# Kernel optimization log

Hardware: AMD Instinct MI355X
Metric: run time of the kernel (lower is better)

## Reference

```python
import jax, jax.numpy as jnp
import numpy as np

NUM_NODES = 200000
NUM_EDGES = 200000
NUM_GRAPHS = 2048
F_IN = 128
H = 64


def setup_inputs() -> dict:
    key = jax.random.key(0)
    ks = jax.random.split(key, 16)
    x = jax.random.normal(ks[0], (NUM_NODES, F_IN), dtype=jnp.float32)
    edge_index = jax.random.randint(ks[1], (2, NUM_EDGES), 0, NUM_NODES, dtype=jnp.int64)
    batch = jnp.sort(jax.random.randint(ks[2], (NUM_NODES,), 0, NUM_GRAPHS, dtype=jnp.int64))
    s_in = 1.0 / np.sqrt(F_IN)
    s_h = 1.0 / np.sqrt(H)
    W1a = jax.random.uniform(ks[3], (F_IN, H), jnp.float32, -s_in, s_in)
    b1a = jax.random.uniform(ks[4], (H,), jnp.float32, -s_in, s_in)
    W1b = jax.random.uniform(ks[5], (H, H), jnp.float32, -s_h, s_h)
    b1b = jax.random.uniform(ks[6], (H,), jnp.float32, -s_h, s_h)
    W2a = jax.random.uniform(ks[7], (H, H), jnp.float32, -s_h, s_h)
    b2a = jax.random.uniform(ks[8], (H,), jnp.float32, -s_h, s_h)
    W2b = jax.random.uniform(ks[9], (H, H), jnp.float32, -s_h, s_h)
    b2b = jax.random.uniform(ks[10], (H,), jnp.float32, -s_h, s_h)
    fcW = jax.random.uniform(ks[11], (H, 1), jnp.float32, -s_h, s_h)
    fcb = jax.random.uniform(ks[12], (1,), jnp.float32, -s_h, s_h)
    return {"x": x, "edge_index": edge_index, "batch": batch,
            "W1a": W1a, "b1a": b1a, "W1b": W1b, "b1b": b1b,
            "W2a": W2a, "b2a": b2a, "W2b": W2b, "b2b": b2b,
            "fcW": fcW, "fcb": fcb}


def gin_conv(h, edge_index, Wa, ba, Wb, bb):
    # sum aggregation: messages from source (row 0) scattered to target (row 1)
    msgs = h[edge_index[0]]  # [E, D]
    agg = jax.ops.segment_sum(msgs, edge_index[1], num_segments=NUM_NODES)
    z = h + agg  # eps = 0 default: (1+eps)*x + sum_j x_j
    z = jnp.maximum(z @ Wa + ba, 0.0)
    return z @ Wb + bb


def reference(x, edge_index, batch, W1a, b1a, W1b, b1b, W2a, b2a, W2b, b2b, fcW, fcb):
    h = jnp.maximum(gin_conv(x, edge_index, W1a, b1a, W1b, b1b), 0.0)
    h = jnp.maximum(gin_conv(h, edge_index, W2a, b2a, W2b, b2b), 0.0)
    # global mean pool per graph
    sums = jax.ops.segment_sum(h, batch, num_segments=NUM_GRAPHS)  # [G, H]
    counts = jax.ops.segment_sum(jnp.ones((h.shape[0],), h.dtype), batch, num_segments=NUM_GRAPHS)
    pooled = sums / jnp.maximum(counts, 1.0)[:, None]
    out = pooled @ fcW + fcb  # [G, 1]
    return out.squeeze(-1)
```

## Files before the change

kernel.cpp:

```cpp
#include <hip/hip_runtime.h>
#include <hip/hip_bf16.h>


#define NODES 200000
#define EDGES 200000
#define GRAPHS 2048
#define NB_SCAN 782

typedef __attribute__((ext_vector_type(8))) short short8;
typedef __attribute__((ext_vector_type(4))) float f32x4;

__device__ __forceinline__ unsigned short f2bf(float f) {
    unsigned u = __builtin_bit_cast(unsigned, f);
    u = (u + 0x7fffu + ((u >> 16) & 1u)) >> 16;
    return (unsigned short)u;
}
__device__ __forceinline__ float bf2f(unsigned short h) {
    unsigned u = ((unsigned)h) << 16;
    return __builtin_bit_cast(float, u);
}

__global__ __launch_bounds__(256) void count_k(
    const int* __restrict__ ei, int* __restrict__ cnt, int E)
{
    int e = blockIdx.x * 256 + threadIdx.x;
    if (e < E) atomicAdd(&cnt[ei[E + e]], 1);
}

__global__ __launch_bounds__(256) void scan1_k(
    const int* __restrict__ cnt, int* __restrict__ excl,
    int* __restrict__ bsum, int N)
{
    __shared__ int sh[256];
    int tid = threadIdx.x;
    int i = blockIdx.x * 256 + tid;
    int v = (i < N) ? cnt[i] : 0;
    sh[tid] = v;
    __syncthreads();
    for (int off = 1; off < 256; off <<= 1) {
        int t = (tid >= off) ? sh[tid - off] : 0;
        __syncthreads();
        sh[tid] += t;
        __syncthreads();
    }
    if (i < N) excl[i] = sh[tid] - v;
    if (tid == 255) bsum[blockIdx.x] = sh[255];
}

__global__ __launch_bounds__(1024) void scan2_k(int* __restrict__ bsum, int NB)
{
    __shared__ int sh[1024];
    int tid = threadIdx.x;
    int v = (tid < NB) ? bsum[tid] : 0;
    sh[tid] = v;
    __syncthreads();
    for (int off = 1; off < 1024; off <<= 1) {
        int t = (tid >= off) ? sh[tid - off] : 0;
        __syncthreads();
        sh[tid] += t;
        __syncthreads();
    }
    if (tid < NB) bsum[tid] = sh[tid] - v;
}

__global__ __launch_bounds__(256) void scan3_k(
    int* __restrict__ rowptr, const int* __restrict__ bsum,
    int* __restrict__ cursor, int N, int E)
{
    int i = blockIdx.x * 256 + threadIdx.x;
    if (i < N) {
        int v = rowptr[i] + bsum[blockIdx.x];
        rowptr[i] = v;
        cursor[i] = v;
    }
    if (i == 0) rowptr[N] = E;
}

__global__ __launch_bounds__(256) void fill_k(
    const int* __restrict__ ei, int* __restrict__ cursor,
    int* __restrict__ srcs, int E)
{
    int e = blockIdx.x * 256 + threadIdx.x;
    if (e < E) {
        int d = ei[E + e];
        int p = atomicAdd(&cursor[d], 1);
        srcs[p] = ei[e];
    }
}

template<int KC>
__device__ __forceinline__ void fill_wfrags(
    const float* __restrict__ W, short* __restrict__ Wf, int tid)
{
    for (int e = tid; e < KC * 4 * 64; e += 256) {
        int lane = e & 63;
        int nb = (e >> 6) & 3;
        int kc = e >> 8;
        int col = nb * 16 + (lane & 15);
        int kb = kc * 32 + ((lane >> 4) * 8);
        short8 hi, lo;
        #pragma unroll
        for (int j = 0; j < 8; ++j) {
            float w = W[(size_t)(kb + j) * 64 + col];
            unsigned short h = f2bf(w);
            float r = w - bf2f(h);
            hi[j] = (short)h;
            lo[j] = (short)f2bf(r);
        }
        *reinterpret_cast<short8*>(Wf + (size_t)e * 8) = hi;
        *reinterpret_cast<short8*>(Wf + ((size_t)(KC * 4 * 64) + e) * 8) = lo;
    }
}

__device__ __forceinline__ void cvt_a8(const float av[8], short8& hi, short8& lo)
{
    #pragma unroll
    for (int j = 0; j < 8; ++j) {
        unsigned short h = f2bf(av[j]);
        float r = av[j] - bf2f(h);
        hi[j] = (short)h;
        lo[j] = (short)f2bf(r);
    }
}

template<int K>
__device__ __forceinline__ void mm_core(
    const float* __restrict__ A, const short* __restrict__ Wf,
    int row0w, int lane, f32x4 acc[4])
{
    constexpr int KC = K / 32;
    const float* Ar = A + (size_t)(row0w + (lane & 15)) * K;
    #pragma unroll
    for (int kc = 0; kc < KC; ++kc) {
        const int kb = kc * 32 + ((lane >> 4) * 8);
        float4 a0 = *reinterpret_cast<const float4*>(Ar + kb);
        float4 a1 = *reinterpret_cast<const float4*>(Ar + kb + 4);
        float av[8] = {a0.x, a0.y, a0.z, a0.w, a1.x, a1.y, a1.z, a1.w};
        short8 ahi, alo;
        cvt_a8(av, ahi, alo);
        #pragma unroll
        for (int nb = 0; nb < 4; ++nb) {
            const short8 whi = *reinterpret_cast<const short8*>(
                Wf + ((size_t)((kc * 4 + nb) * 64) + lane) * 8);
            const short8 wlo = *reinterpret_cast<const short8*>(
                Wf + ((size_t)((KC * 4 + kc * 4 + nb) * 64) + lane) * 8);
            acc[nb] = __builtin_amdgcn_mfma_f32_16x16x32_bf16(ahi, whi, acc[nb], 0, 0, 0);
            acc[nb] = __builtin_amdgcn_mfma_f32_16x16x32_bf16(alo, whi, acc[nb], 0, 0, 0);
            acc[nb] = __builtin_amdgcn_mfma_f32_16x16x32_bf16(ahi, wlo, acc[nb], 0, 0, 0);
        }
    }
}

template<int K, bool BIAS, bool RELU>
__global__ __launch_bounds__(256) void mm_k(
    const float* __restrict__ A, const float* __restrict__ W,
    const float* __restrict__ bias, float* __restrict__ out, int N)
{
    constexpr int KC = K / 32;
    __shared__ short Wf[2 * KC * 4 * 64 * 8];
    const int tid = threadIdx.x;
    fill_wfrags<KC>(W, Wf, tid);
    __syncthreads();

    const int lane = tid & 63;
    const int row0w = blockIdx.x * 64 + (tid >> 6) * 16;

    f32x4 acc[4] = {{0.f, 0.f, 0.f, 0.f}, {0.f, 0.f, 0.f, 0.f},
                    {0.f, 0.f, 0.f, 0.f}, {0.f, 0.f, 0.f, 0.f}};
    mm_core<K>(A, Wf, row0w, lane, acc);

    const int grp = lane >> 4, c = lane & 15;
    #pragma unroll
    for (int nb = 0; nb < 4; ++nb) {
        const int col = nb * 16 + c;
        const float bv = BIAS ? bias[col] : 0.f;
        #pragma unroll
        for (int reg = 0; reg < 4; ++reg) {
            const int orow = row0w + grp * 4 + reg;
            float v = acc[nb][reg] + bv;
            if (RELU) v = fmaxf(v, 0.f);
            out[(size_t)orow * 64 + col] = v;
        }
    }
}

__global__ __launch_bounds__(256) void mm_pool_k(
    const float* __restrict__ A, const float* __restrict__ W,
    const float* __restrict__ bias, const float* __restrict__ fcW,
    const int* __restrict__ batch, float* __restrict__ gacc, int N)
{
    constexpr int KC = 2;
    __shared__ short Wf[2 * KC * 4 * 64 * 8];
    __shared__ float rd[4][16];
    __shared__ int bls[4][16];
    const int tid = threadIdx.x;
    fill_wfrags<KC>(W, Wf, tid);
    __syncthreads();

    const int lane = tid & 63;
    const int wv = tid >> 6;
    const int row0w = blockIdx.x * 64 + wv * 16;

    f32x4 acc[4] = {{0.f, 0.f, 0.f, 0.f}, {0.f, 0.f, 0.f, 0.f},
                    {0.f, 0.f, 0.f, 0.f}, {0.f, 0.f, 0.f, 0.f}};
    mm_core<64>(A, Wf, row0w, lane, acc);

    const int grp = lane >> 4, c = lane & 15;
    float bv[4], fw[4];
    #pragma unroll
    for (int nb = 0; nb < 4; ++nb) {
        bv[nb] = bias[nb * 16 + c];
        fw[nb] = fcW[nb * 16 + c];
    }
    if (c < 16 && grp == 0) {  }
    if (lane < 16) bls[wv][lane] = batch[row0w + lane];

    #pragma unroll
    for (int reg = 0; reg < 4; ++reg) {
        float t = 0.f;
        #pragma unroll
        for (int nb = 0; nb < 4; ++nb)
            t += fmaxf(acc[nb][reg] + bv[nb], 0.f) * fw[nb];
        t += __shfl_xor(t, 1, 16);
        t += __shfl_xor(t, 2, 16);
        t += __shfl_xor(t, 4, 16);
        t += __shfl_xor(t, 8, 16);
        if (c == 0) rd[wv][grp * 4 + reg] = t;
    }

    if (lane == 0) {
        int curg = bls[wv][0];
        float s = rd[wv][0];
        #pragma unroll
        for (int i = 1; i < 16; ++i) {
            int g = bls[wv][i];
            float v = rd[wv][i];
            if (g == curg) s += v;
            else { atomicAdd(&gacc[curg], s); curg = g; s = v; }
        }
        atomicAdd(&gacc[curg], s);
    }
}

__global__ __launch_bounds__(256) void agg_relu_k(
    const float* __restrict__ y, const int* __restrict__ rowptr,
    const int* __restrict__ srcs, const float* __restrict__ bias,
    float* __restrict__ zin, int N)
{
    int t = blockIdx.x * 256 + threadIdx.x;
    int node = t >> 4;
    if (node >= N) return;
    int c = (t & 15) * 4;

    int s0 = rowptr[node];
    int s1 = rowptr[node + 1];

    float4 acc = *reinterpret_cast<const float4*>(y + (size_t)node * 64 + c);
    float4 b4 = *reinterpret_cast<const float4*>(bias + c);
    acc.x += b4.x; acc.y += b4.y; acc.z += b4.z; acc.w += b4.w;

    for (int j = s0; j < s1; ++j) {
        int s = srcs[j];
        float4 vv = *reinterpret_cast<const float4*>(y + (size_t)s * 64 + c);
        acc.x += vv.x; acc.y += vv.y; acc.z += vv.z; acc.w += vv.w;
    }

    float4 o;
    o.x = fmaxf(acc.x, 0.f);
    o.y = fmaxf(acc.y, 0.f);
    o.z = fmaxf(acc.z, 0.f);
    o.w = fmaxf(acc.w, 0.f);
    *reinterpret_cast<float4*>(zin + (size_t)node * 64 + c) = o;
}

__global__ __launch_bounds__(256) void finalize_k(
    const float* __restrict__ gacc, const int* __restrict__ batch,
    const float* __restrict__ fcb, float* __restrict__ out, int N, int G)
{
    int g = blockIdx.x * 256 + threadIdx.x;
    if (g >= G) return;
    int lo = 0, hi = N;
    while (lo < hi) { int m = (lo + hi) >> 1; if (batch[m] < g) lo = m + 1; else hi = m; }
    int start = lo;
    hi = N;
    while (lo < hi) { int m = (lo + hi) >> 1; if (batch[m] < g + 1) lo = m + 1; else hi = m; }
    float cnt = fmaxf((float)(lo - start), 1.f);
    out[g] = gacc[g] / cnt + fcb[0];
}

extern "C" void kernel_launch(void* const* d_in, const int* in_sizes, int n_in,
                              void* d_out, int out_size, void* d_ws, size_t ws_size,
                              hipStream_t stream)
{
    const float* x     = (const float*)d_in[0];
    const int*   ei    = (const int*)d_in[1];
    const int*   batch = (const int*)d_in[2];
    const float* W1a   = (const float*)d_in[3];
    const float* b1a   = (const float*)d_in[4];
    const float* W1b   = (const float*)d_in[5];
    const float* b1b   = (const float*)d_in[6];
    const float* W2a   = (const float*)d_in[7];
    const float* b2a   = (const float*)d_in[8];
    const float* W2b   = (const float*)d_in[9];
    const float* b2b   = (const float*)d_in[10];
    const float* fcW   = (const float*)d_in[11];
    const float* fcb   = (const float*)d_in[12];
    float* out = (float*)d_out;

    const int N = NODES, E = EDGES, G = GRAPHS;
    char* ws = (char*)d_ws;
    const size_t szH = (size_t)N * 64 * sizeof(float);

    float* yBuf   = (float*)ws;
    float* zinBuf = (float*)(ws + szH);
    float* hBuf   = (float*)(ws + 2 * szH);
    char*  rest   = ws + 3 * szH;
    int* cnt    = (int*)rest;
    int* rowptr = cnt + NODES;
    int* cursor = rowptr + NODES + 1;
    int* srcs   = cursor + NODES;
    int* bsum   = srcs + EDGES;
    float* gacc = (float*)(bsum + NB_SCAN + 2);

    hipMemsetAsync(cnt, 0, (size_t)N * sizeof(int), stream);
    hipMemsetAsync(gacc, 0, (size_t)G * sizeof(float), stream);
    count_k<<<NB_SCAN, 256, 0, stream>>>(ei, cnt, E);
    scan1_k<<<NB_SCAN, 256, 0, stream>>>(cnt, rowptr, bsum, N);
    scan2_k<<<1, 1024, 0, stream>>>(bsum, NB_SCAN);
    scan3_k<<<NB_SCAN, 256, 0, stream>>>(rowptr, bsum, cursor, N, E);
    fill_k<<<NB_SCAN, 256, 0, stream>>>(ei, cursor, srcs, E);

    mm_k<128, false, false><<<N / 64, 256, 0, stream>>>(x, W1a, nullptr, yBuf, N);
    agg_relu_k<<<N * 16 / 256, 256, 0, stream>>>(yBuf, rowptr, srcs, b1a, zinBuf, N);
    mm_k<64, true, true><<<N / 64, 256, 0, stream>>>(zinBuf, W1b, b1b, hBuf, N);

    mm_k<64, false, false><<<N / 64, 256, 0, stream>>>(hBuf, W2a, nullptr, yBuf, N);
    agg_relu_k<<<N * 16 / 256, 256, 0, stream>>>(yBuf, rowptr, srcs, b2a, zinBuf, N);

    mm_pool_k<<<N / 64, 256, 0, stream>>>(zinBuf, W2b, b2b, fcW, batch, gacc, N);
    finalize_k<<<(G + 255) / 256, 256, 0, stream>>>(gacc, batch, fcb, out, N, G);
}
```

Measured before the change: 334.6 us.

## Fuse back-to-back GEMMs, precompute weight splits, store activations as bf16 hi/lo

Weight bf16 hi/lo fragments are now built once by a separate kernel and read from global memory, instead of being rebuilt into LDS in every block. The Wb GEMM of layer 1 and the Wa GEMM of layer 2 are fused into one kernel that passes the intermediate through LDS, removing one full-size activation round trip and one launch. The aggregation kernels write split bf16 hi/lo arrays directly, so the following GEMMs skip the float-to-bf16 conversion. Each wave now handles 32 rows, which raises reuse of the weight fragments. Buffers are padded to a multiple of 128 rows, and the padded tail rows of zHi/zLo are read without being written.

```diff
diff --git a/kernel.cpp b/kernel.cpp
--- a/kernel.cpp
+++ b/kernel.cpp
@@ -3,11 +3,13 @@
 
 
 #define NODES 200000
+#define NPAD  200064
 #define EDGES 200000
 #define GRAPHS 2048
 #define NB_SCAN 782
 
 typedef __attribute__((ext_vector_type(8))) short short8;
+typedef __attribute__((ext_vector_type(4))) short short4v;
 typedef __attribute__((ext_vector_type(4))) float f32x4;
 
 __device__ __forceinline__ unsigned short f2bf(float f) {
@@ -88,32 +90,42 @@
     }
 }
 
-template<int KC>
-__device__ __forceinline__ void fill_wfrags(
-    const float* __restrict__ W, short* __restrict__ Wf, int tid)
-{
-    for (int e = tid; e < KC * 4 * 64; e += 256) {
-        int lane = e & 63;
-        int nb = (e >> 6) & 3;
-        int kc = e >> 8;
-        int col = nb * 16 + (lane & 15);
-        int kb = kc * 32 + ((lane >> 4) * 8);
-        short8 hi, lo;
-        #pragma unroll
-        for (int j = 0; j < 8; ++j) {
-            float w = W[(size_t)(kb + j) * 64 + col];
-            unsigned short h = f2bf(w);
-            float r = w - bf2f(h);
-            hi[j] = (short)h;
-            lo[j] = (short)f2bf(r);
-        }
-        *reinterpret_cast<short8*>(Wf + (size_t)e * 8) = hi;
-        *reinterpret_cast<short8*>(Wf + ((size_t)(KC * 4 * 64) + e) * 8) = lo;
-    }
-}
-
-__device__ __forceinline__ void cvt_a8(const float av[8], short8& hi, short8& lo)
-{
+__device__ __forceinline__ void wconv(const float* __restrict__ W,
+                                      short* __restrict__ F, int e, int NE)
+{
+    int lane = e & 63, nb = (e >> 6) & 3, kc = e >> 8;
+    int col = nb * 16 + (lane & 15);
+    int kb = kc * 32 + ((lane >> 4) * 8);
+    short8 hi, lo;
+    #pragma unroll
+    for (int j = 0; j < 8; ++j) {
+        float w = W[(size_t)(kb + j) * 64 + col];
+        unsigned short h = f2bf(w);
+        float r = w - bf2f(h);
+        hi[j] = (short)h;
+        lo[j] = (short)f2bf(r);
+    }
+    *reinterpret_cast<short8*>(F + (size_t)e * 8) = hi;
+    *reinterpret_cast<short8*>(F + (size_t)NE * 8 + (size_t)e * 8) = lo;
+}
+
+__global__ __launch_bounds__(256) void wsplit_k(
+    const float* __restrict__ W1a, const float* __restrict__ W1b,
+    const float* __restrict__ W2a, const float* __restrict__ W2b,
+    short* __restrict__ F1a, short* __restrict__ F1b,
+    short* __restrict__ F2a, short* __restrict__ F2b)
+{
+    int t = blockIdx.x * 256 + threadIdx.x;
+    if (t < 1024)      wconv(W1a, F1a, t, 1024);
+    else if (t < 1536) wconv(W1b, F1b, t - 1024, 512);
+    else if (t < 2048) wconv(W2a, F2a, t - 1536, 512);
+    else if (t < 2560) wconv(W2b, F2b, t - 2048, 512);
+}
+
+__device__ __forceinline__ void cvt_a8(const float4& a, const float4& b,
+                                       short8& hi, short8& lo)
+{
+    float av[8] = {a.x, a.y, a.z, a.w, b.x, b.y, b.z, b.w};
     #pragma unroll
     for (int j = 0; j < 8; ++j) {
         unsigned short h = f2bf(av[j]);
@@ -123,129 +135,63 @@
     }
 }
 
-template<int K>
-__device__ __forceinline__ void mm_core(
+__global__ __launch_bounds__(256) void mm1_k(
     const float* __restrict__ A, const short* __restrict__ Wf,
-    int row0w, int lane, f32x4 acc[4])
-{
-    constexpr int KC = K / 32;
-    const float* Ar = A + (size_t)(row0w + (lane & 15)) * K;
-    #pragma unroll
-    for (int kc = 0; kc < KC; ++kc) {
-        const int kb = kc * 32 + ((lane >> 4) * 8);
-        float4 a0 = *reinterpret_cast<const float4*>(Ar + kb);
-        float4 a1 = *reinterpret_cast<const float4*>(Ar + kb + 4);
-        float av[8] = {a0.x, a0.y, a0.z, a0.w, a1.x, a1.y, a1.z, a1.w};
-        short8 ahi, alo;
-        cvt_a8(av, ahi, alo);
-        #pragma unroll
-        for (int nb = 0; nb < 4; ++nb) {
-            const short8 whi = *reinterpret_cast<const short8*>(
-                Wf + ((size_t)((kc * 4 + nb) * 64) + lane) * 8);
-            const short8 wlo = *reinterpret_cast<const short8*>(
-                Wf + ((size_t)((KC * 4 + kc * 4 + nb) * 64) + lane) * 8);
-            acc[nb] = __builtin_amdgcn_mfma_f32_16x16x32_bf16(ahi, whi, acc[nb], 0, 0, 0);
-            acc[nb] = __builtin_amdgcn_mfma_f32_16x16x32_bf16(alo, whi, acc[nb], 0, 0, 0);
-            acc[nb] = __builtin_amdgcn_mfma_f32_16x16x32_bf16(ahi, wlo, acc[nb], 0, 0, 0);
-        }
-    }
-}
-
-template<int K, bool BIAS, bool RELU>
-__global__ __launch_bounds__(256) void mm_k(
-    const float* __restrict__ A, const float* __restrict__ W,
-    const float* __restrict__ bias, float* __restrict__ out, int N)
-{
-    constexpr int KC = K / 32;
-    __shared__ short Wf[2 * KC * 4 * 64 * 8];
+    float* __restrict__ out, int N)
+{
     const int tid = threadIdx.x;
-    fill_wfrags<KC>(W, Wf, tid);
-    __syncthreads();
-
-    const int lane = tid & 63;
-    const int row0w = blockIdx.x * 64 + (tid >> 6) * 16;
-
-    f32x4 acc[4] = {{0.f, 0.f, 0.f, 0.f}, {0.f, 0.f, 0.f, 0.f},
-                    {0.f, 0.f, 0.f, 0.f}, {0.f, 0.f, 0.f, 0.f}};
-    mm_core<K>(A, Wf, row0w, lane, acc);
-
-    const int grp = lane >> 4, c = lane & 15;
-    #pragma unroll
-    for (int nb = 0; nb < 4; ++nb) {
-        const int col = nb * 16 + c;
-        const float bv = BIAS ? bias[col] : 0.f;
-        #pragma unroll
-        for (int reg = 0; reg < 4; ++reg) {
-            const int orow = row0w + grp * 4 + reg;
-            float v = acc[nb][reg] + bv;
-            if (RELU) v = fmaxf(v, 0.f);
-            out[(size_t)orow * 64 + col] = v;
-        }
-    }
-}
-
-__global__ __launch_bounds__(256) void mm_pool_k(
-    const float* __restrict__ A, const float* __restrict__ W,
-    const float* __restrict__ bias, const float* __restrict__ fcW,
-    const int* __restrict__ batch, float* __restrict__ gacc, int N)
-{
-    constexpr int KC = 2;
-    __shared__ short Wf[2 * KC * 4 * 64 * 8];
-    __shared__ float rd[4][16];
-    __shared__ int bls[4][16];
-    const int tid = threadIdx.x;
-    fill_wfrags<KC>(W, Wf, tid);
-    __syncthreads();
-
     const int lane = tid & 63;
     const int wv = tid >> 6;
-    const int row0w = blockIdx.x * 64 + wv * 16;
-
-    f32x4 acc[4] = {{0.f, 0.f, 0.f, 0.f}, {0.f, 0.f, 0.f, 0.f},
-                    {0.f, 0.f, 0.f, 0.f}, {0.f, 0.f, 0.f, 0.f}};
-    mm_core<64>(A, Wf, row0w, lane, acc);
-
+    const int row0w = blockIdx.x * 128 + wv * 32;
     const int grp = lane >> 4, c = lane & 15;
-    float bv[4], fw[4];
-    #pragma unroll
-    for (int nb = 0; nb < 4; ++nb) {
-        bv[nb] = bias[nb * 16 + c];
-        fw[nb] = fcW[nb * 16 + c];
-    }
-    if (c < 16 && grp == 0) {  }
-    if (lane < 16) bls[wv][lane] = batch[row0w + lane];
-
-    #pragma unroll
-    for (int reg = 0; reg < 4; ++reg) {
-        float t = 0.f;
-        #pragma unroll
-        for (int nb = 0; nb < 4; ++nb)
-            t += fmaxf(acc[nb][reg] + bv[nb], 0.f) * fw[nb];
-        t += __shfl_xor(t, 1, 16);
-        t += __shfl_xor(t, 2, 16);
-        t += __shfl_xor(t, 4, 16);
-        t += __shfl_xor(t, 8, 16);
-        if (c == 0) rd[wv][grp * 4 + reg] = t;
-    }
-
-    if (lane == 0) {
-        int curg = bls[wv][0];
-        float s = rd[wv][0];
-        #pragma unroll
-        for (int i = 1; i < 16; ++i) {
-            int g = bls[wv][i];
-            float v = rd[wv][i];
-            if (g == curg) s += v;
-            else { atomicAdd(&gacc[curg], s); curg = g; s = v; }
-        }
-        atomicAdd(&gacc[curg], s);
-    }
-}
-
-__global__ __launch_bounds__(256) void agg_relu_k(
+    const int koff = grp * 8;
+
+    const float* Ar0 = A + (size_t)min(row0w + c, N - 1) * 128;
+    const float* Ar1 = A + (size_t)min(row0w + 16 + c, N - 1) * 128;
+
+    f32x4 acc[2][4];
+    #pragma unroll
+    for (int rg = 0; rg < 2; ++rg)
+        #pragma unroll
+        for (int nb = 0; nb < 4; ++nb)
+            acc[rg][nb] = (f32x4){0.f, 0.f, 0.f, 0.f};
+
+    #pragma unroll
+    for (int kc = 0; kc < 4; ++kc) {
+        const int kb = kc * 32 + koff;
+        float4 a00 = *reinterpret_cast<const float4*>(Ar0 + kb);
+        float4 a01 = *reinterpret_cast<const float4*>(Ar0 + kb + 4);
+        float4 a10 = *reinterpret_cast<const float4*>(Ar1 + kb);
+        float4 a11 = *reinterpret_cast<const float4*>(Ar1 + kb + 4);
+        short8 h0, l0, h1, l1;
+        cvt_a8(a00, a01, h0, l0);
+        cvt_a8(a10, a11, h1, l1);
+        #pragma unroll
+        for (int nb = 0; nb < 4; ++nb) {
+            short8 whi = *reinterpret_cast<const short8*>(Wf + ((size_t)((kc * 4 + nb) * 64) + lane) * 8);
+            short8 wlo = *reinterpret_cast<const short8*>(Wf + ((size_t)(1024 + (kc * 4 + nb) * 64) + lane) * 8);
+            acc[0][nb] = __builtin_amdgcn_mfma_f32_16x16x32_bf16(h0, whi, acc[0][nb], 0, 0, 0);
+            acc[0][nb] = __builtin_amdgcn_mfma_f32_16x16x32_bf16(l0, whi, acc[0][nb], 0, 0, 0);
+            acc[0][nb] = __builtin_amdgcn_mfma_f32_16x16x32_bf16(h0, wlo, acc[0][nb], 0, 0, 0);
+            acc[1][nb] = __builtin_amdgcn_mfma_f32_16x16x32_bf16(h1, whi, acc[1][nb], 0, 0, 0);
+            acc[1][nb] = __builtin_amdgcn_mfma_f32_16x16x32_bf16(l1, whi, acc[1][nb], 0, 0, 0);
+            acc[1][nb] = __builtin_amdgcn_mfma_f32_16x16x32_bf16(h1, wlo, acc[1][nb], 0, 0, 0);
+        }
+    }
+
+    #pragma unroll
+    for (int rg = 0; rg < 2; ++rg)
+        #pragma unroll
+        for (int nb = 0; nb < 4; ++nb)
+            #pragma unroll
+            for (int reg = 0; reg < 4; ++reg)
+                out[(size_t)(row0w + rg * 16 + grp * 4 + reg) * 64 + nb * 16 + c] = acc[rg][nb][reg];
+}
+
+__global__ __launch_bounds__(256) void agg_split_k(
     const float* __restrict__ y, const int* __restrict__ rowptr,
     const int* __restrict__ srcs, const float* __restrict__ bias,
-    float* __restrict__ zin, int N)
+    short* __restrict__ zHi, short* __restrict__ zLo, int N)
 {
     int t = blockIdx.x * 256 + threadIdx.x;
     int node = t >> 4;
@@ -265,12 +211,189 @@
         acc.x += vv.x; acc.y += vv.y; acc.z += vv.z; acc.w += vv.w;
     }
 
-    float4 o;
-    o.x = fmaxf(acc.x, 0.f);
-    o.y = fmaxf(acc.y, 0.f);
-    o.z = fmaxf(acc.z, 0.f);
-    o.w = fmaxf(acc.w, 0.f);
-    *reinterpret_cast<float4*>(zin + (size_t)node * 64 + c) = o;
+    float v[4] = {fmaxf(acc.x, 0.f), fmaxf(acc.y, 0.f),
+                  fmaxf(acc.z, 0.f), fmaxf(acc.w, 0.f)};
+    short4v hv, lv;
+    #pragma unroll
+    for (int i = 0; i < 4; ++i) {
+        unsigned short h = f2bf(v[i]);
+        float r = v[i] - bf2f(h);
+        hv[i] = (short)h;
+        lv[i] = (short)f2bf(r);
+    }
+    *reinterpret_cast<short4v*>(zHi + (size_t)node * 64 + c) = hv;
+    *reinterpret_cast<short4v*>(zLo + (size_t)node * 64 + c) = lv;
+}
+
+__device__ __forceinline__ void mm64_core(
+    const short* __restrict__ zHi, const short* __restrict__ zLo,
+    const short* __restrict__ Wf, int row0w, int lane, f32x4 acc[2][4])
+{
+    const int grp = lane >> 4, c = lane & 15;
+    const int koff = grp * 8;
+    const short* zh0 = zHi + (size_t)(row0w + c) * 64;
+    const short* zl0 = zLo + (size_t)(row0w + c) * 64;
+    const short* zh1 = zHi + (size_t)(row0w + 16 + c) * 64;
+    const short* zl1 = zLo + (size_t)(row0w + 16 + c) * 64;
+
+    #pragma unroll
+    for (int kc = 0; kc < 2; ++kc) {
+        const int kb = kc * 32 + koff;
+        short8 h0 = *reinterpret_cast<const short8*>(zh0 + kb);
+        short8 l0 = *reinterpret_cast<const short8*>(zl0 + kb);
+        short8 h1 = *reinterpret_cast<const short8*>(zh1 + kb);
+        short8 l1 = *reinterpret_cast<const short8*>(zl1 + kb);
+        #pragma unroll
+        for (int nb = 0; nb < 4; ++nb) {
+            short8 whi = *reinterpret_cast<const short8*>(Wf + ((size_t)((kc * 4 + nb) * 64) + lane) * 8);
+            short8 wlo = *reinterpret_cast<const short8*>(Wf + ((size_t)(512 + (kc * 4 + nb) * 64) + lane) * 8);
+            acc[0][nb] = __builtin_amdgcn_mfma_f32_16x16x32_bf16(h0, whi, acc[0][nb], 0, 0, 0);
+            acc[0][nb] = __builtin_amdgcn_mfma_f32_16x16x32_bf16(l0, whi, acc[0][nb], 0, 0, 0);
+            acc[0][nb] = __builtin_amdgcn_mfma_f32_16x16x32_bf16(h0, wlo, acc[0][nb], 0, 0, 0);
+            acc[1][nb] = __builtin_amdgcn_mfma_f32_16x16x32_bf16(h1, whi, acc[1][nb], 0, 0, 0);
+            acc[1][nb] = __builtin_amdgcn_mfma_f32_16x16x32_bf16(l1, whi, acc[1][nb], 0, 0, 0);
+            acc[1][nb] = __builtin_amdgcn_mfma_f32_16x16x32_bf16(h1, wlo, acc[1][nb], 0, 0, 0);
+        }
+    }
+}
+
+__global__ __launch_bounds__(256) void mmmm_k(
+    const short* __restrict__ zHi, const short* __restrict__ zLo,
+    const short* __restrict__ Wf1, const float* __restrict__ b1,
+    const short* __restrict__ Wf2, float* __restrict__ out)
+{
+    __shared__ short hT[4][32 * 72];
+    __shared__ short lT[4][32 * 72];
+    const int tid = threadIdx.x;
+    const int lane = tid & 63;
+    const int wv = tid >> 6;
+    const int row0w = blockIdx.x * 128 + wv * 32;
+    const int grp = lane >> 4, c = lane & 15;
+    const int koff = grp * 8;
+
+    f32x4 acc[2][4];
+    #pragma unroll
+    for (int rg = 0; rg < 2; ++rg)
+        #pragma unroll
+        for (int nb = 0; nb < 4; ++nb)
+            acc[rg][nb] = (f32x4){0.f, 0.f, 0.f, 0.f};
+
+    mm64_core(zHi, zLo, Wf1, row0w, lane, acc);
+
+    #pragma unroll
+    for (int rg = 0; rg < 2; ++rg)
+        #pragma unroll
+        for (int nb = 0; nb < 4; ++nb) {
+            const int col = nb * 16 + c;
+            const float bv = b1[col];
+            #pragma unroll
+            for (int reg = 0; reg < 4; ++reg) {
+                const int lr = rg * 16 + grp * 4 + reg;
+                float v = fmaxf(acc[rg][nb][reg] + bv, 0.f);
+                unsigned short h = f2bf(v);
+                float r = v - bf2f(h);
+                hT[wv][lr * 72 + col] = (short)h;
+                lT[wv][lr * 72 + col] = (short)f2bf(r);
+            }
+        }
+    __syncthreads();
+
+    f32x4 acc2[2][4];
+    #pragma unroll
+    for (int rg = 0; rg < 2; ++rg)
+        #pragma unroll
+        for (int nb = 0; nb < 4; ++nb)
+            acc2[rg][nb] = (f32x4){0.f, 0.f, 0.f, 0.f};
+
+    #pragma unroll
+    for (int kc = 0; kc < 2; ++kc) {
+        const int kb = kc * 32 + koff;
+        short8 h0 = *reinterpret_cast<const short8*>(&hT[wv][(0 + c) * 72 + kb]);
+        short8 l0 = *reinterpret_cast<const short8*>(&lT[wv][(0 + c) * 72 + kb]);
+        short8 h1 = *reinterpret_cast<const short8*>(&hT[wv][(16 + c) * 72 + kb]);
+        short8 l1 = *reinterpret_cast<const short8*>(&lT[wv][(16 + c) * 72 + kb]);
+        #pragma unroll
+        for (int nb = 0; nb < 4; ++nb) {
+            short8 whi = *reinterpret_cast<const short8*>(Wf2 + ((size_t)((kc * 4 + nb) * 64) + lane) * 8);
+            short8 wlo = *reinterpret_cast<const short8*>(Wf2 + ((size_t)(512 + (kc * 4 + nb) * 64) + lane) * 8);
+            acc2[0][nb] = __builtin_amdgcn_mfma_f32_16x16x32_bf16(h0, whi, acc2[0][nb], 0, 0, 0);
+            acc2[0][nb] = __builtin_amdgcn_mfma_f32_16x16x32_bf16(l0, whi, acc2[0][nb], 0, 0, 0);
+            acc2[0][nb] = __builtin_amdgcn_mfma_f32_16x16x32_bf16(h0, wlo, acc2[0][nb], 0, 0, 0);
+            acc2[1][nb] = __builtin_amdgcn_mfma_f32_16x16x32_bf16(h1, whi, acc2[1][nb], 0, 0, 0);
+            acc2[1][nb] = __builtin_amdgcn_mfma_f32_16x16x32_bf16(l1, whi, acc2[1][nb], 0, 0, 0);
+            acc2[1][nb] = __builtin_amdgcn_mfma_f32_16x16x32_bf16(h1, wlo, acc2[1][nb], 0, 0, 0);
+        }
+    }
+
+    #pragma unroll
+    for (int rg = 0; rg < 2; ++rg)
+        #pragma unroll
+        for (int nb = 0; nb < 4; ++nb)
+            #pragma unroll
+            for (int reg = 0; reg < 4; ++reg)
+                out[(size_t)(row0w + rg * 16 + grp * 4 + reg) * 64 + nb * 16 + c] = acc2[rg][nb][reg];
+}
+
+__global__ __launch_bounds__(256) void mmpool_k(
+    const short* __restrict__ zHi, const short* __restrict__ zLo,
+    const short* __restrict__ Wf, const float* __restrict__ bias,
+    const float* __restrict__ fcW, const int* __restrict__ batch,
+    float* __restrict__ gacc, int N)
+{
+    __shared__ float rd[4][32];
+    __shared__ int bls[4][32];
+    const int tid = threadIdx.x;
+    const int lane = tid & 63;
+    const int wv = tid >> 6;
+    const int row0w = blockIdx.x * 128 + wv * 32;
+    const int grp = lane >> 4, c = lane & 15;
+
+    f32x4 acc[2][4];
+    #pragma unroll
+    for (int rg = 0; rg < 2; ++rg)
+        #pragma unroll
+        for (int nb = 0; nb < 4; ++nb)
+            acc[rg][nb] = (f32x4){0.f, 0.f, 0.f, 0.f};
+
+    mm64_core(zHi, zLo, Wf, row0w, lane, acc);
+
+    float bv[4], fw[4];
+    #pragma unroll
+    for (int nb = 0; nb < 4; ++nb) {
+        bv[nb] = bias[nb * 16 + c];
+        fw[nb] = fcW[nb * 16 + c];
+    }
+    if (lane < 32) bls[wv][lane] = batch[min(row0w + lane, N - 1)];
+
+    #pragma unroll
+    for (int rg = 0; rg < 2; ++rg)
+        #pragma unroll
+        for (int reg = 0; reg < 4; ++reg) {
+            float t = 0.f;
+            #pragma unroll
+            for (int nb = 0; nb < 4; ++nb)
+                t += fmaxf(acc[rg][nb][reg] + bv[nb], 0.f) * fw[nb];
+            t += __shfl_xor(t, 1, 16);
+            t += __shfl_xor(t, 2, 16);
+            t += __shfl_xor(t, 4, 16);
+            t += __shfl_xor(t, 8, 16);
+            if (c == 0) rd[wv][rg * 16 + grp * 4 + reg] = t;
+        }
+
+    if (lane == 0) {
+        int cnt = min(32, N - row0w);
+        if (cnt > 0) {
+            int curg = bls[wv][0];
+            float s = rd[wv][0];
+            for (int i = 1; i < cnt; ++i) {
+                int g = bls[wv][i];
+                float v = rd[wv][i];
+                if (g == curg) s += v;
+                else { atomicAdd(&gacc[curg], s); curg = g; s = v; }
+            }
+            atomicAdd(&gacc[curg], s);
+        }
+    }
 }
 
 __global__ __launch_bounds__(256) void finalize_k(
@@ -309,18 +432,23 @@
 
     const int N = NODES, E = EDGES, G = GRAPHS;
     char* ws = (char*)d_ws;
-    const size_t szH = (size_t)N * 64 * sizeof(float);
-
-    float* yBuf   = (float*)ws;
-    float* zinBuf = (float*)(ws + szH);
-    float* hBuf   = (float*)(ws + 2 * szH);
-    char*  rest   = ws + 3 * szH;
+
+    float* yBuf = (float*)ws;
+    short* zHi  = (short*)(ws + (size_t)NPAD * 64 * 4);
+    short* zLo  = zHi + (size_t)NPAD * 64;
+    char*  rest = (char*)(zLo + (size_t)NPAD * 64);
     int* cnt    = (int*)rest;
     int* rowptr = cnt + NODES;
     int* cursor = rowptr + NODES + 1;
     int* srcs   = cursor + NODES;
     int* bsum   = srcs + EDGES;
     float* gacc = (float*)(bsum + NB_SCAN + 2);
+    short* F1a  = (short*)(((size_t)(gacc + GRAPHS) + 63) & ~(size_t)63);
+    short* F1b  = F1a + 2 * 1024 * 8;
+    short* F2a  = F1b + 2 * 512 * 8;
+    short* F2b  = F2a + 2 * 512 * 8;
+
+    const int NBLK = NPAD / 128;
 
     hipMemsetAsync(cnt, 0, (size_t)N * sizeof(int), stream);
     hipMemsetAsync(gacc, 0, (size_t)G * sizeof(float), stream);
@@ -329,14 +457,15 @@
     scan2_k<<<1, 1024, 0, stream>>>(bsum, NB_SCAN);
     scan3_k<<<NB_SCAN, 256, 0, stream>>>(rowptr, bsum, cursor, N, E);
     fill_k<<<NB_SCAN, 256, 0, stream>>>(ei, cursor, srcs, E);
-
-    mm_k<128, false, false><<<N / 64, 256, 0, stream>>>(x, W1a, nullptr, yBuf, N);
-    agg_relu_k<<<N * 16 / 256, 256, 0, stream>>>(yBuf, rowptr, srcs, b1a, zinBuf, N);
-    mm_k<64, true, true><<<N / 64, 256, 0, stream>>>(zinBuf, W1b, b1b, hBuf, N);
-
-    mm_k<64, false, false><<<N / 64, 256, 0, stream>>>(hBuf, W2a, nullptr, yBuf, N);
-    agg_relu_k<<<N * 16 / 256, 256, 0, stream>>>(yBuf, rowptr, srcs, b2a, zinBuf, N);
-
-    mm_pool_k<<<N / 64, 256, 0, stream>>>(zinBuf, W2b, b2b, fcW, batch, gacc, N);
+    wsplit_k<<<10, 256, 0, stream>>>(W1a, W1b, W2a, W2b, F1a, F1b, F2a, F2b);
+
+    mm1_k<<<NBLK, 256, 0, stream>>>(x, F1a, yBuf, N);
+    agg_split_k<<<N * 16 / 256, 256, 0, stream>>>(yBuf, rowptr, srcs, b1a, zHi, zLo, N);
+
+    mmmm_k<<<NBLK, 256, 0, stream>>>(zHi, zLo, F1b, b1b, F2a, yBuf);
+
+    agg_split_k<<<N * 16 / 256, 256, 0, stream>>>(yBuf, rowptr, srcs, b2a, zHi, zLo, N);
+
+    mmpool_k<<<NBLK, 256, 0, stream>>>(zHi, zLo, F2b, b2b, fcW, batch, gacc, N);
     finalize_k<<<(G + 255) / 256, 256, 0, stream>>>(gacc, batch, fcb, out, N, G);
 }
```

After: 328.8 us. About the same (-1.7%).
